# Kernel tuning notes

Measured on AMD Instinct MI355X. Metric: run time of the kernel, lower is better.

Reference implementation:

```python
import jax, jax.numpy as jnp
import numpy as np

RADIUS = 0.2
NSAMPLE = 32
BANDWIDTH = 0.1


def ellipsoid_query(xyz, new_xyz, radius, nsample):
    """xyz:(B,N,3), new_xyz:(B,P,3) -> idx:(B,P,nsample) int32.
    Ellipsoid semi-axes (radius, 2*radius, radius); first nsample hits,
    padded with the first hit (index 0 if empty), matching the CUDA kernel.
    """
    B, N, _ = xyz.shape
    inv_sq = jnp.asarray([1.0 / radius**2, 1.0 / (2.0 * radius) ** 2, 1.0 / radius**2],
                         dtype=xyz.dtype)
    # accumulate per-coordinate to avoid a (B,P,N,3) intermediate
    q = jnp.zeros((B, new_xyz.shape[1], N), dtype=xyz.dtype)
    for k in range(3):
        d = new_xyz[:, :, None, k] - xyz[:, None, :, k]  # (B,P,N)
        q = q + d * d * inv_sq[k]
    mask = q < 1.0
    cand = jnp.where(mask, jnp.arange(N, dtype=jnp.int32), jnp.int32(N))  # invalid -> N
    cand = jnp.sort(cand, axis=-1)[..., :nsample]                          # (B,P,S)
    first = cand[..., :1]
    first = jnp.where(first >= N, jnp.int32(0), first)
    return jnp.where(cand >= N, first, cand)


def group(features, idx):
    """features:(B,C,N), idx:(B,P,S) -> (B,C,P,S)"""
    return jnp.take_along_axis(features[:, :, None, :], idx[:, None, :, :], axis=-1)


def setup_inputs() -> dict:
    key = jax.random.key(0)
    k1, k2, k3 = jax.random.split(key, 3)
    xyz = jax.random.uniform(k1, (4, 8192, 3), dtype=jnp.float32)
    new_xyz = jax.random.uniform(k2, (4, 2048, 3), dtype=jnp.float32)
    features = jax.random.normal(k3, (4, 64, 8192), dtype=jnp.float32)
    return {"xyz": xyz, "new_xyz": new_xyz, "features": features}


def reference(xyz, new_xyz, features):
    idx = ellipsoid_query(xyz, new_xyz, RADIUS, NSAMPLE)          # (B,P,S)
    xyz_trans = jnp.transpose(xyz, (0, 2, 1))                      # (B,3,N)
    grouped_xyz = group(xyz_trans, idx)                            # (B,3,P,S)
    # density: gaussian of distance to center
    g = jnp.transpose(grouped_xyz, (0, 2, 3, 1))                   # (B,P,S,3)
    dist = jnp.linalg.norm(g - new_xyz[:, :, None, :], axis=-1)    # (B,P,S)
    density = jnp.exp(-dist**2 / (2.0 * BANDWIDTH**2)) / (2.5 * BANDWIDTH)
    grouped_density = (1.0 / density)[:, None, :, :]               # (B,1,P,S)
    grouped_features = group(features, idx)                        # (B,C,P,S)
    return jnp.concatenate([grouped_xyz, grouped_density, grouped_features], axis=1)
```

## Files before the change

kernel.cpp:

```cpp
#include <hip/hip_runtime.h>

constexpr int NPTS = 8192;
constexpr int NQ   = 2048;
constexpr int NC   = 64;
constexpr int NS   = 32;
constexpr int NCH  = 3 + 1 + NC;
constexpr int CS   = NQ * NS;


__global__ __launch_bounds__(256, 8) void prep_kernel(
    const float* __restrict__ feat,
    const float* __restrict__ xyz,
    float* __restrict__ ftr,
    float* __restrict__ soa)
{
    const int b  = blockIdx.y;
    const int bx = blockIdx.x;
    const int t  = threadIdx.x;

    if (bx < NPTS / 64) {
        __shared__ float tile[NC][65];
        const int n0 = bx * 64;
        const float* fb = feat + (size_t)b * NC * NPTS;
        {
            const int pl = t & 63;
            const int c0 = t >> 6;
            #pragma unroll
            for (int i = 0; i < 16; ++i) {
                const int c = c0 + 4 * i;
                tile[c][pl] = fb[(size_t)c * NPTS + n0 + pl];
            }
        }
        __syncthreads();
        float* tb = ftr + ((size_t)b * NPTS + n0) * NC;
        {
            const int cl = t & 63;
            const int pb = t >> 6;
            #pragma unroll
            for (int i = 0; i < 16; ++i) {
                const int pp = pb + 4 * i;
                tb[(size_t)pp * NC + cl] = tile[cl][pp];
            }
        }
    } else {
        const int n0 = (bx - NPTS / 64) * 4096;
        const float* xb = xyz + (size_t)b * NPTS * 3;
        float* xs = soa + (size_t)b * 3 * NPTS;
        float* ys = xs + NPTS;
        float* zs = ys + NPTS;
        #pragma unroll
        for (int k = 0; k < 16; ++k) {
            const int i = n0 + k * 256 + t;
            xs[i] = xb[i * 3 + 0];
            ys[i] = xb[i * 3 + 1];
            zs[i] = xb[i * 3 + 2];
        }
    }
}

__global__ __launch_bounds__(256, 8) void scan_kernel(
    const float* __restrict__ soa,
    const float* __restrict__ nxyz,
    int* __restrict__ gidx,
    float* __restrict__ out)
{
    __shared__ int idx_s[4][NS];

    const int b    = blockIdx.y;
    const int tid  = threadIdx.x;
    const int lane = tid & 63;
    const int wave = tid >> 6;
    const int p    = blockIdx.x * 4 + wave;

    const float* xs = soa + (size_t)b * 3 * NPTS;
    const float* ys = xs + NPTS;
    const float* zs = ys + NPTS;
    int* idx_row = idx_s[wave];

    const float qx = nxyz[((size_t)b * NQ + p) * 3 + 0];
    const float qy = nxyz[((size_t)b * NQ + p) * 3 + 1];
    const float qz = nxyz[((size_t)b * NQ + p) * 3 + 2];

    int cnt = 0;
    int first = -1;

    float x0 = xs[lane],      y0 = ys[lane],      z0 = zs[lane];
    float x1 = xs[64 + lane], y1 = ys[64 + lane], z1 = zs[64 + lane];

    for (int base = 0; base < NPTS; base += 64) {
        float xn = 0.f, yn = 0.f, zn = 0.f;
        const int pf = base + 128;
        if (pf < NPTS) {
            xn = xs[pf + lane]; yn = ys[pf + lane]; zn = zs[pf + lane];
        }

        const float dx = __fsub_rn(qx, x0);
        const float dy = __fsub_rn(qy, y0);
        const float dz = __fsub_rn(qz, z0);
        const float t0 = __fmul_rn(__fmul_rn(dx, dx), 25.0f);
        const float t1 = __fmul_rn(__fmul_rn(dy, dy), 6.25f);
        const float t2 = __fmul_rn(__fmul_rn(dz, dz), 25.0f);
        const float qv = __fadd_rn(__fadd_rn(t0, t1), t2);
        const bool hit = qv < 1.0f;

        const unsigned long long m = __ballot(hit);
        if (first < 0 && m != 0ull)
            first = base + __builtin_ctzll(m);
        if (hit) {
            const int pos = cnt + __popcll(m & ((1ull << lane) - 1ull));
            if (pos < NS) idx_row[pos] = base + lane;
        }
        cnt += __popcll(m);
        if (cnt >= NS) break;

        x0 = x1; y0 = y1; z0 = z1;
        x1 = xn; y1 = yn; z1 = zn;
    }
    if (cnt < NS) {
        const int f = (cnt == 0) ? 0 : first;
        if (lane < NS && lane >= cnt) idx_row[lane] = f;
    }

    if (lane < NS) {
        const int s = lane;
        const int j = idx_row[s];
        gidx[((size_t)b * NQ + p) * NS + s] = j;

        const float px = xs[j], py = ys[j], pz = zs[j];
        const float dx = __fsub_rn(px, qx);
        const float dy = __fsub_rn(py, qy);
        const float dz = __fsub_rn(pz, qz);
        const float d2 = __fadd_rn(__fadd_rn(__fmul_rn(dx, dx), __fmul_rn(dy, dy)),
                                   __fmul_rn(dz, dz));
        const float dist = __fsqrt_rn(d2);
        const float arg  = __fdiv_rn(-__fmul_rn(dist, dist), 0.02f);
        const float density = __fmul_rn(expf(arg), 4.0f);
        const float gd = __fdiv_rn(1.0f, density);

        float* ob = out + ((size_t)b * NCH * NQ + p) * NS + s;
        ob[0 * (size_t)CS] = px;
        ob[1 * (size_t)CS] = py;
        ob[2 * (size_t)CS] = pz;
        ob[3 * (size_t)CS] = gd;
    }
}

__global__ __launch_bounds__(512, 8) void group_kernel(
    const int* __restrict__ gidx,
    const float* __restrict__ ftr,
    float* __restrict__ out,
    int B)
{
    __shared__ float ldsc[NC][33];

    const int g = blockIdx.x;
    int b, p;
    if (B == 4) {
        b = (g & 7) >> 1;
        p = ((g >> 3) << 1) | (g & 1);
    } else {
        b = g / NQ;
        p = g - b * NQ;
    }
    const int tid = threadIdx.x;

    const int cg = tid & 15;
    const int sl = tid >> 4;
    const int j  = gidx[((size_t)b * NQ + p) * NS + sl];
    const float4 v = ((const float4*)(ftr + ((size_t)b * NPTS + j) * NC))[cg];
    ldsc[4 * cg + 0][sl] = v.x;
    ldsc[4 * cg + 1][sl] = v.y;
    ldsc[4 * cg + 2][sl] = v.z;
    ldsc[4 * cg + 3][sl] = v.w;
    __syncthreads();

    const int c  = tid >> 3;
    const int s4 = (tid & 7) << 2;
    float4 w;
    w.x = ldsc[c][s4 + 0];
    w.y = ldsc[c][s4 + 1];
    w.z = ldsc[c][s4 + 2];
    w.w = ldsc[c][s4 + 3];
    float* op = out + (((size_t)b * NCH + 4 + c) * NQ + p) * NS + s4;
    *(float4*)op = w;
}

__global__ __launch_bounds__(512, 8) void ellip_direct_kernel(
    const float* __restrict__ xyz,
    const float* __restrict__ nxyz,
    const float* __restrict__ feat,
    float* __restrict__ out)
{
    __shared__ int idx_s[8][NS];

    const int b    = blockIdx.y;
    const int p0   = blockIdx.x * 8;
    const int tid  = threadIdx.x;
    const int lane = tid & 63;
    const int wave = tid >> 6;
    const float* xb = xyz + (size_t)b * NPTS * 3;

    {
        const int p = p0 + wave;
        const float qx = nxyz[((size_t)b * NQ + p) * 3 + 0];
        const float qy = nxyz[((size_t)b * NQ + p) * 3 + 1];
        const float qz = nxyz[((size_t)b * NQ + p) * 3 + 2];
        int cnt = 0, first = -1;
        for (int base = 0; base < NPTS; base += 64) {
            const int i = base + lane;
            const float dx = __fsub_rn(qx, xb[i * 3 + 0]);
            const float dy = __fsub_rn(qy, xb[i * 3 + 1]);
            const float dz = __fsub_rn(qz, xb[i * 3 + 2]);
            const float t0 = __fmul_rn(__fmul_rn(dx, dx), 25.0f);
            const float t1 = __fmul_rn(__fmul_rn(dy, dy), 6.25f);
            const float t2 = __fmul_rn(__fmul_rn(dz, dz), 25.0f);
            const float qv = __fadd_rn(__fadd_rn(t0, t1), t2);
            const bool hit = qv < 1.0f;
            const unsigned long long m = __ballot(hit);
            if (first < 0 && m != 0ull) first = base + __builtin_ctzll(m);
            if (hit) {
                const int pos = cnt + __popcll(m & ((1ull << lane) - 1ull));
                if (pos < NS) idx_s[wave][pos] = i;
            }
            cnt += __popcll(m);
            if (cnt >= NS) break;
        }
        if (cnt < NS) {
            const int f = (cnt == 0) ? 0 : first;
            if (lane < NS && lane >= cnt) idx_s[wave][lane] = f;
        }
    }
    __syncthreads();

    const int s = tid & 31;
    const int h = (tid >> 5) & 1;
    const int q = tid >> 6;
    const int p = p0 + q;
    const int j = idx_s[q][s];
    float* ob = out + ((size_t)b * NCH * NQ + p) * NS + s;

    if (h == 0) {
        const float qx = nxyz[((size_t)b * NQ + p) * 3 + 0];
        const float qy = nxyz[((size_t)b * NQ + p) * 3 + 1];
        const float qz = nxyz[((size_t)b * NQ + p) * 3 + 2];
        const float px = xb[j * 3 + 0], py = xb[j * 3 + 1], pz = xb[j * 3 + 2];
        const float dx = __fsub_rn(px, qx);
        const float dy = __fsub_rn(py, qy);
        const float dz = __fsub_rn(pz, qz);
        const float d2 = __fadd_rn(__fadd_rn(__fmul_rn(dx, dx), __fmul_rn(dy, dy)),
                                   __fmul_rn(dz, dz));
        const float dist = __fsqrt_rn(d2);
        const float arg  = __fdiv_rn(-__fmul_rn(dist, dist), 0.02f);
        const float gd = __fdiv_rn(1.0f, __fmul_rn(expf(arg), 4.0f));
        ob[0 * (size_t)CS] = px;
        ob[1 * (size_t)CS] = py;
        ob[2 * (size_t)CS] = pz;
        ob[3 * (size_t)CS] = gd;
    }
    const float* fb = feat + (size_t)b * NC * NPTS + j;
    #pragma unroll 4
    for (int c = h; c < NC; c += 2)
        ob[(size_t)(4 + c) * CS] = fb[(size_t)c * NPTS];
}

extern "C" void kernel_launch(void* const* d_in, const int* in_sizes, int n_in,
                              void* d_out, int out_size, void* d_ws, size_t ws_size,
                              hipStream_t stream) {
    const float* xyz  = (const float*)d_in[0];
    const float* nxyz = (const float*)d_in[1];
    const float* feat = (const float*)d_in[2];
    float* out = (float*)d_out;

    const int B = in_sizes[0] / (NPTS * 3);
    const size_t ftr_f = (size_t)B * NPTS * NC;
    const size_t soa_f = (size_t)B * 3 * NPTS;
    const size_t idx_f = (size_t)B * NQ * NS;
    const size_t need  = (ftr_f + soa_f + idx_f) * 4;

    if (ws_size >= need) {
        float* ftr = (float*)d_ws;
        float* soa = ftr + ftr_f;
        int*   idx = (int*)(soa + soa_f);

        prep_kernel<<<dim3(NPTS / 64 + 2, B), 256, 0, stream>>>(feat, xyz, ftr, soa);
        scan_kernel<<<dim3(NQ / 4, B), 256, 0, stream>>>(soa, nxyz, idx, out);
        group_kernel<<<dim3(B * NQ), 512, 0, stream>>>(idx, ftr, out, B);
    } else {
        ellip_direct_kernel<<<dim3(NQ / 8, B), 512, 0, stream>>>(xyz, nxyz, feat, out);
    }
}
```

Before: 112.2 us.

## Fuse feature transpose and ball scan into one kernel with LDS-staged points

Merges the prep (feature transpose + xyz AoS-to-SoA) and scan kernels into a single 1024-thread launch. Transpose blocks and scan blocks share the grid, and the SoA workspace is removed. Each scan block stages the first 4096 points of xyz in LDS and serves 16 queries from it, falling back to global AoS loads for the remaining points. This removes a kernel launch and the SoA round-trip, in exchange for large LDS use that limits occupancy and strided global loads in the tail path.

```diff
diff --git a/kernel.cpp b/kernel.cpp
--- a/kernel.cpp
+++ b/kernel.cpp
@@ -6,97 +6,85 @@
 constexpr int NS   = 32;
 constexpr int NCH  = 3 + 1 + NC;
 constexpr int CS   = NQ * NS;
-
-
-__global__ __launch_bounds__(256, 8) void prep_kernel(
+constexpr int LPTS = 4096;
+constexpr int QPB2 = 16;
+
+
+struct ScanLds { float pts[3][LPTS]; int idx[QPB2][NS]; };
+union  KLds    { ScanLds s; float tile[2][NC][65]; };
+
+__global__ __launch_bounds__(1024, 8) void scan_trans_kernel(
+    const float* __restrict__ xyz,
+    const float* __restrict__ nxyz,
     const float* __restrict__ feat,
-    const float* __restrict__ xyz,
     float* __restrict__ ftr,
-    float* __restrict__ soa)
+    int* __restrict__ gidx,
+    float* __restrict__ out,
+    int ntrans)
 {
-    const int b  = blockIdx.y;
+    __shared__ KLds u;
     const int bx = blockIdx.x;
     const int t  = threadIdx.x;
 
-    if (bx < NPTS / 64) {
-        __shared__ float tile[NC][65];
-        const int n0 = bx * 64;
+    if (bx < ntrans) {
+        const int b   = bx >> 6;
+        const int tl2 = bx & 63;
+        const int h   = t >> 9;
+        const int v   = t & 511;
+        const int pl  = v & 63;
+        const int c0  = v >> 6;
+        const int n0  = tl2 * 128 + h * 64;
         const float* fb = feat + (size_t)b * NC * NPTS;
-        {
-            const int pl = t & 63;
-            const int c0 = t >> 6;
-            #pragma unroll
-            for (int i = 0; i < 16; ++i) {
-                const int c = c0 + 4 * i;
-                tile[c][pl] = fb[(size_t)c * NPTS + n0 + pl];
-            }
+        #pragma unroll
+        for (int i = 0; i < 8; ++i) {
+            const int c = c0 + 8 * i;
+            u.tile[h][c][pl] = fb[(size_t)c * NPTS + n0 + pl];
         }
         __syncthreads();
         float* tb = ftr + ((size_t)b * NPTS + n0) * NC;
-        {
-            const int cl = t & 63;
-            const int pb = t >> 6;
-            #pragma unroll
-            for (int i = 0; i < 16; ++i) {
-                const int pp = pb + 4 * i;
-                tb[(size_t)pp * NC + cl] = tile[cl][pp];
-            }
-        }
-    } else {
-        const int n0 = (bx - NPTS / 64) * 4096;
-        const float* xb = xyz + (size_t)b * NPTS * 3;
-        float* xs = soa + (size_t)b * 3 * NPTS;
-        float* ys = xs + NPTS;
-        float* zs = ys + NPTS;
         #pragma unroll
-        for (int k = 0; k < 16; ++k) {
-            const int i = n0 + k * 256 + t;
-            xs[i] = xb[i * 3 + 0];
-            ys[i] = xb[i * 3 + 1];
-            zs[i] = xb[i * 3 + 2];
-        }
-    }
-}
-
-__global__ __launch_bounds__(256, 8) void scan_kernel(
-    const float* __restrict__ soa,
-    const float* __restrict__ nxyz,
-    int* __restrict__ gidx,
-    float* __restrict__ out)
-{
-    __shared__ int idx_s[4][NS];
-
-    const int b    = blockIdx.y;
-    const int tid  = threadIdx.x;
-    const int lane = tid & 63;
-    const int wave = tid >> 6;
-    const int p    = blockIdx.x * 4 + wave;
-
-    const float* xs = soa + (size_t)b * 3 * NPTS;
-    const float* ys = xs + NPTS;
-    const float* zs = ys + NPTS;
-    int* idx_row = idx_s[wave];
-
+        for (int i = 0; i < 8; ++i) {
+            const int pp = c0 + 8 * i;
+            tb[(size_t)pp * NC + pl] = u.tile[h][pl][pp];
+        }
+        return;
+    }
+
+    const int sb   = bx - ntrans;
+    const int qpb  = NQ / QPB2;
+    const int b    = sb / qpb;
+    const int p0   = (sb - b * qpb) * QPB2;
+    const int lane = t & 63;
+    const int wave = t >> 6;
+    const float* xb = xyz + (size_t)b * NPTS * 3;
+
+    #pragma unroll
+    for (int k = 0; k < 3 * LPTS / 1024; ++k) {
+        const int g  = k * 1024 + t;
+        const float val = xb[g];
+        const int pt = g / 3;
+        const int c  = g - 3 * pt;
+        u.s.pts[c][pt] = val;
+    }
+    __syncthreads();
+
+    const int p = p0 + wave;
     const float qx = nxyz[((size_t)b * NQ + p) * 3 + 0];
     const float qy = nxyz[((size_t)b * NQ + p) * 3 + 1];
     const float qz = nxyz[((size_t)b * NQ + p) * 3 + 2];
 
     int cnt = 0;
     int first = -1;
-
-    float x0 = xs[lane],      y0 = ys[lane],      z0 = zs[lane];
-    float x1 = xs[64 + lane], y1 = ys[64 + lane], z1 = zs[64 + lane];
-
-    for (int base = 0; base < NPTS; base += 64) {
-        float xn = 0.f, yn = 0.f, zn = 0.f;
-        const int pf = base + 128;
-        if (pf < NPTS) {
-            xn = xs[pf + lane]; yn = ys[pf + lane]; zn = zs[pf + lane];
-        }
-
-        const float dx = __fsub_rn(qx, x0);
-        const float dy = __fsub_rn(qy, y0);
-        const float dz = __fsub_rn(qz, z0);
+    int* idx_row = u.s.idx[wave];
+
+    for (int base = 0; base < LPTS; base += 64) {
+        const int i = base + lane;
+        const float x = u.s.pts[0][i];
+        const float y = u.s.pts[1][i];
+        const float z = u.s.pts[2][i];
+        const float dx = __fsub_rn(qx, x);
+        const float dy = __fsub_rn(qy, y);
+        const float dz = __fsub_rn(qz, z);
         const float t0 = __fmul_rn(__fmul_rn(dx, dx), 25.0f);
         const float t1 = __fmul_rn(__fmul_rn(dy, dy), 6.25f);
         const float t2 = __fmul_rn(__fmul_rn(dz, dz), 25.0f);
@@ -108,14 +96,50 @@
             first = base + __builtin_ctzll(m);
         if (hit) {
             const int pos = cnt + __popcll(m & ((1ull << lane) - 1ull));
-            if (pos < NS) idx_row[pos] = base + lane;
+            if (pos < NS) idx_row[pos] = i;
         }
         cnt += __popcll(m);
         if (cnt >= NS) break;
-
-        x0 = x1; y0 = y1; z0 = z1;
-        x1 = xn; y1 = yn; z1 = zn;
-    }
+    }
+
+    if (cnt < NS) {
+        float x0 = xb[3 * (LPTS + lane) + 0];
+        float y0 = xb[3 * (LPTS + lane) + 1];
+        float z0 = xb[3 * (LPTS + lane) + 2];
+        float x1 = xb[3 * (LPTS + 64 + lane) + 0];
+        float y1 = xb[3 * (LPTS + 64 + lane) + 1];
+        float z1 = xb[3 * (LPTS + 64 + lane) + 2];
+        for (int base = LPTS; base < NPTS; base += 64) {
+            float xn = 0.f, yn = 0.f, zn = 0.f;
+            const int pf = base + 128;
+            if (pf < NPTS) {
+                xn = xb[3 * (pf + lane) + 0];
+                yn = xb[3 * (pf + lane) + 1];
+                zn = xb[3 * (pf + lane) + 2];
+            }
+            const float dx = __fsub_rn(qx, x0);
+            const float dy = __fsub_rn(qy, y0);
+            const float dz = __fsub_rn(qz, z0);
+            const float t0 = __fmul_rn(__fmul_rn(dx, dx), 25.0f);
+            const float t1 = __fmul_rn(__fmul_rn(dy, dy), 6.25f);
+            const float t2 = __fmul_rn(__fmul_rn(dz, dz), 25.0f);
+            const float qv = __fadd_rn(__fadd_rn(t0, t1), t2);
+            const bool hit = qv < 1.0f;
+
+            const unsigned long long m = __ballot(hit);
+            if (first < 0 && m != 0ull)
+                first = base + __builtin_ctzll(m);
+            if (hit) {
+                const int pos = cnt + __popcll(m & ((1ull << lane) - 1ull));
+                if (pos < NS) idx_row[pos] = base + lane;
+            }
+            cnt += __popcll(m);
+            if (cnt >= NS) break;
+            x0 = x1; y0 = y1; z0 = z1;
+            x1 = xn; y1 = yn; z1 = zn;
+        }
+    }
+
     if (cnt < NS) {
         const int f = (cnt == 0) ? 0 : first;
         if (lane < NS && lane >= cnt) idx_row[lane] = f;
@@ -126,7 +150,9 @@
         const int j = idx_row[s];
         gidx[((size_t)b * NQ + p) * NS + s] = j;
 
-        const float px = xs[j], py = ys[j], pz = zs[j];
+        const float px = xb[3 * j + 0];
+        const float py = xb[3 * j + 1];
+        const float pz = xb[3 * j + 2];
         const float dx = __fsub_rn(px, qx);
         const float dy = __fsub_rn(py, qy);
         const float dz = __fsub_rn(pz, qz);
@@ -273,17 +299,17 @@
 
     const int B = in_sizes[0] / (NPTS * 3);
     const size_t ftr_f = (size_t)B * NPTS * NC;
-    const size_t soa_f = (size_t)B * 3 * NPTS;
     const size_t idx_f = (size_t)B * NQ * NS;
-    const size_t need  = (ftr_f + soa_f + idx_f) * 4;
+    const size_t need  = (ftr_f + idx_f) * 4;
 
     if (ws_size >= need) {
         float* ftr = (float*)d_ws;
-        float* soa = ftr + ftr_f;
-        int*   idx = (int*)(soa + soa_f);
-
-        prep_kernel<<<dim3(NPTS / 64 + 2, B), 256, 0, stream>>>(feat, xyz, ftr, soa);
-        scan_kernel<<<dim3(NQ / 4, B), 256, 0, stream>>>(soa, nxyz, idx, out);
+        int*   idx = (int*)(ftr + ftr_f);
+
+        const int ntrans = B * 64;
+        const int nscan  = B * (NQ / QPB2);
+        scan_trans_kernel<<<dim3(ntrans + nscan), 1024, 0, stream>>>(
+            xyz, nxyz, feat, ftr, idx, out, ntrans);
         group_kernel<<<dim3(B * NQ), 512, 0, stream>>>(idx, ftr, out, B);
     } else {
         ellip_direct_kernel<<<dim3(NQ / 8, B), 512, 0, stream>>>(xyz, nxyz, feat, out);
```

Result: faster. 102.7 us (-8.5%).

## Fuse feature transpose and ellipsoid scan into one launch, drop SoA conversion

Applied to the files above, without the earlier changes.

Merges the prep kernel (feature transpose plus xyz AoS-to-SoA) and the scan kernel into a single launch whose blocks are split by index between transpose work and query scanning. The scan now reads xyz directly in interleaved AoS layout, which removes the SoA buffer and one kernel launch. It also replaces the masked popcount with mbcnt intrinsics for the prefix count. In exchange, the scan's loads become strided (stride 3), which may be less coalesced than the earlier unit-stride SoA reads.

```diff
diff --git a/kernel.cpp b/kernel.cpp
--- a/kernel.cpp
+++ b/kernel.cpp
@@ -8,19 +8,34 @@
 constexpr int CS   = NQ * NS;
 
 
-__global__ __launch_bounds__(256, 8) void prep_kernel(
+
+union KLds {
+    float tile[NC][65];
+    int   idx[4][NS];
+};
+
+__device__ __forceinline__ unsigned prefix_popc(unsigned long long m) {
+    return __builtin_amdgcn_mbcnt_hi((unsigned)(m >> 32),
+           __builtin_amdgcn_mbcnt_lo((unsigned)m, 0u));
+}
+
+__global__ __launch_bounds__(256, 8) void scan_trans_kernel(
+    const float* __restrict__ xyz,
+    const float* __restrict__ nxyz,
     const float* __restrict__ feat,
-    const float* __restrict__ xyz,
     float* __restrict__ ftr,
-    float* __restrict__ soa)
+    int* __restrict__ gidx,
+    float* __restrict__ out,
+    int ntrans)
 {
-    const int b  = blockIdx.y;
+    __shared__ KLds u;
     const int bx = blockIdx.x;
     const int t  = threadIdx.x;
 
-    if (bx < NPTS / 64) {
-        __shared__ float tile[NC][65];
-        const int n0 = bx * 64;
+    if (bx < ntrans) {
+        const int b  = bx >> 7;
+        const int tl = bx & 127;
+        const int n0 = tl * 64;
         const float* fb = feat + (size_t)b * NC * NPTS;
         {
             const int pl = t & 63;
@@ -28,7 +43,7 @@
             #pragma unroll
             for (int i = 0; i < 16; ++i) {
                 const int c = c0 + 4 * i;
-                tile[c][pl] = fb[(size_t)c * NPTS + n0 + pl];
+                u.tile[c][pl] = fb[(size_t)c * NPTS + n0 + pl];
             }
         }
         __syncthreads();
@@ -39,43 +54,21 @@
             #pragma unroll
             for (int i = 0; i < 16; ++i) {
                 const int pp = pb + 4 * i;
-                tb[(size_t)pp * NC + cl] = tile[cl][pp];
+                tb[(size_t)pp * NC + cl] = u.tile[cl][pp];
             }
         }
-    } else {
-        const int n0 = (bx - NPTS / 64) * 4096;
-        const float* xb = xyz + (size_t)b * NPTS * 3;
-        float* xs = soa + (size_t)b * 3 * NPTS;
-        float* ys = xs + NPTS;
-        float* zs = ys + NPTS;
-        #pragma unroll
-        for (int k = 0; k < 16; ++k) {
-            const int i = n0 + k * 256 + t;
-            xs[i] = xb[i * 3 + 0];
-            ys[i] = xb[i * 3 + 1];
-            zs[i] = xb[i * 3 + 2];
-        }
-    }
-}
-
-__global__ __launch_bounds__(256, 8) void scan_kernel(
-    const float* __restrict__ soa,
-    const float* __restrict__ nxyz,
-    int* __restrict__ gidx,
-    float* __restrict__ out)
-{
-    __shared__ int idx_s[4][NS];
-
-    const int b    = blockIdx.y;
-    const int tid  = threadIdx.x;
-    const int lane = tid & 63;
-    const int wave = tid >> 6;
-    const int p    = blockIdx.x * 4 + wave;
-
-    const float* xs = soa + (size_t)b * 3 * NPTS;
-    const float* ys = xs + NPTS;
-    const float* zs = ys + NPTS;
-    int* idx_row = idx_s[wave];
+        return;
+    }
+
+    const int sb   = bx - ntrans;
+    const int qpb  = NQ / 4;
+    const int b    = sb / qpb;
+    const int p0   = (sb - b * qpb) * 4;
+    const int lane = t & 63;
+    const int wave = t >> 6;
+    const int p    = p0 + wave;
+    const float* xb = xyz + (size_t)b * NPTS * 3;
+    int* idx_row = u.idx[wave];
 
     const float qx = nxyz[((size_t)b * NQ + p) * 3 + 0];
     const float qy = nxyz[((size_t)b * NQ + p) * 3 + 1];
@@ -84,14 +77,17 @@
     int cnt = 0;
     int first = -1;
 
-    float x0 = xs[lane],      y0 = ys[lane],      z0 = zs[lane];
-    float x1 = xs[64 + lane], y1 = ys[64 + lane], z1 = zs[64 + lane];
+    float x0 = xb[3 * lane + 0], y0 = xb[3 * lane + 1], z0 = xb[3 * lane + 2];
+    float x1 = xb[3 * (64 + lane) + 0], y1 = xb[3 * (64 + lane) + 1],
+          z1 = xb[3 * (64 + lane) + 2];
 
     for (int base = 0; base < NPTS; base += 64) {
         float xn = 0.f, yn = 0.f, zn = 0.f;
         const int pf = base + 128;
         if (pf < NPTS) {
-            xn = xs[pf + lane]; yn = ys[pf + lane]; zn = zs[pf + lane];
+            xn = xb[3 * (pf + lane) + 0];
+            yn = xb[3 * (pf + lane) + 1];
+            zn = xb[3 * (pf + lane) + 2];
         }
 
         const float dx = __fsub_rn(qx, x0);
@@ -107,7 +103,7 @@
         if (first < 0 && m != 0ull)
             first = base + __builtin_ctzll(m);
         if (hit) {
-            const int pos = cnt + __popcll(m & ((1ull << lane) - 1ull));
+            const int pos = cnt + (int)prefix_popc(m);
             if (pos < NS) idx_row[pos] = base + lane;
         }
         cnt += __popcll(m);
@@ -126,7 +122,9 @@
         const int j = idx_row[s];
         gidx[((size_t)b * NQ + p) * NS + s] = j;
 
-        const float px = xs[j], py = ys[j], pz = zs[j];
+        const float px = xb[3 * j + 0];
+        const float py = xb[3 * j + 1];
+        const float pz = xb[3 * j + 2];
         const float dx = __fsub_rn(px, qx);
         const float dy = __fsub_rn(py, qy);
         const float dz = __fsub_rn(pz, qz);
@@ -273,17 +271,17 @@
 
     const int B = in_sizes[0] / (NPTS * 3);
     const size_t ftr_f = (size_t)B * NPTS * NC;
-    const size_t soa_f = (size_t)B * 3 * NPTS;
     const size_t idx_f = (size_t)B * NQ * NS;
-    const size_t need  = (ftr_f + soa_f + idx_f) * 4;
+    const size_t need  = (ftr_f + idx_f) * 4;
 
     if (ws_size >= need) {
         float* ftr = (float*)d_ws;
-        float* soa = ftr + ftr_f;
-        int*   idx = (int*)(soa + soa_f);
-
-        prep_kernel<<<dim3(NPTS / 64 + 2, B), 256, 0, stream>>>(feat, xyz, ftr, soa);
-        scan_kernel<<<dim3(NQ / 4, B), 256, 0, stream>>>(soa, nxyz, idx, out);
+        int*   idx = (int*)(ftr + ftr_f);
+
+        const int ntrans = B * (NPTS / 64);
+        const int nscan  = B * (NQ / 4);
+        scan_trans_kernel<<<dim3(ntrans + nscan), 256, 0, stream>>>(
+            xyz, nxyz, feat, ftr, idx, out, ntrans);
         group_kernel<<<dim3(B * NQ), 512, 0, stream>>>(idx, ftr, out, B);
     } else {
         ellip_direct_kernel<<<dim3(NQ / 8, B), 512, 0, stream>>>(xyz, nxyz, feat, out);
```

After: 112.6 us. No clear change (+0.4%).
